# Kernel tuning notes

Measured on AMD Instinct MI355X. Metric: run time of the kernel, lower is better.

Reference implementation:

```python
import jax, jax.numpy as jnp
import numpy as np

IMG = 448; P = 16; C = 3; D = 512; DC = 8; DS = 4
NH = IMG // P            # 28 patches per side
NPATCH = NH * NH         # 784
PDIM = C * P * P         # 768
BATCH = 32
EPS = 1e-5


def setup_inputs() -> dict:
    key = jax.random.key(0)
    ks = jax.random.split(key, 10)
    def lin(k, fan_in, shape):
        bound = 1.0 / np.sqrt(fan_in)
        return jax.random.uniform(k, shape, jnp.float32, -bound, bound)
    return {
        "images": jax.random.normal(ks[0], (BATCH, C, IMG, IMG), jnp.float32),
        "W_patch": lin(ks[1], PDIM, (PDIM, D)),
        "b_patch": jnp.zeros((D,), jnp.float32),
        "pos_embed": jax.random.normal(ks[2], (1, NPATCH, D), jnp.float32) * 0.02,
        "W_coord": lin(ks[3], D, (D, DC)),
        "b_coord": jnp.zeros((DC,), jnp.float32),
        "W_spinor": lin(ks[4], D, (D, DS)),
        "b_spinor": jnp.zeros((DS,), jnp.float32),
        "W_embed": lin(ks[5], DC, (DC, D)),
        "b_embed": jnp.zeros((D,), jnp.float32),
        "ln_gamma": jnp.ones((D,), jnp.float32),
        "ln_beta": jnp.zeros((D,), jnp.float32),
        "W_out": lin(ks[6], D, (D, D)),
        "b_out": jnp.zeros((D,), jnp.float32),
    }


def reference(images, W_patch, b_patch, pos_embed, W_coord, b_coord,
              W_spinor, b_spinor, W_embed, b_embed,
              ln_gamma, ln_beta, W_out, b_out):
    B = images.shape[0]
    # patchify == F.unfold(kernel=stride=P).transpose(1,2):
    # patches[b, bh*NH+bw, c*P*P + i*P + j] = images[b, c, bh*P+i, bw*P+j]
    patches = images.reshape(B, C, NH, P, NH, P)
    patches = patches.transpose(0, 2, 4, 1, 3, 5).reshape(B, NPATCH, PDIM)
    # patch embed + positional embedding  -> (B, NPATCH, D)
    x = patches @ W_patch + b_patch + pos_embed
    # manifold projection: coords (B,N,DC), spinor (B,N,DS)
    coords = x @ W_coord + b_coord
    spinor = x @ W_spinor + b_spinor
    # K0 scalar bilinear: psi^T psi -> (B, N)
    K0 = jnp.sum(spinor * spinor, axis=-1)
    # embed back from manifold coords -> (B, N, D)
    x_manifold = coords @ W_embed + b_embed
    # K0-modulated remix + residual
    x_enh = x_manifold * K0[..., None] + x
    # output projection: LayerNorm -> Linear
    mu = jnp.mean(x_enh, axis=-1, keepdims=True)
    var = jnp.mean(jnp.square(x_enh - mu), axis=-1, keepdims=True)
    x_norm = (x_enh - mu) * jax.lax.rsqrt(var + EPS) * ln_gamma + ln_beta
    return x_norm @ W_out + b_out
```

## Files before the change

kernel.cpp:

```cpp
#include <hip/hip_runtime.h>
#include <hip/hip_bf16.h>
#include <stdint.h>


typedef __bf16 bf16_t;
typedef bf16_t bf16x8 __attribute__((ext_vector_type(8)));
typedef bf16_t bf16x4 __attribute__((ext_vector_type(4)));
typedef float  f32x4  __attribute__((ext_vector_type(4)));

#define IMG     448
#define PSZ     16
#define NHP     28
#define NPATCH  784
#define PDIM    768
#define DMODEL  512
#define MROWS   25088

__device__ __forceinline__ void gload16(void* lds, const void* g) {
  __builtin_amdgcn_global_load_lds(
      (__attribute__((address_space(1))) void*)(uintptr_t)g,
      (__attribute__((address_space(3))) void*)lds,
      16, 0, 0);
}

__global__ __launch_bounds__(256) void prep_patchify(
    const float* __restrict__ Wp, const float* __restrict__ Wo,
    const float* __restrict__ Wc, const float* __restrict__ Ws,
    const float* __restrict__ images,
    bf16_t* __restrict__ WpT, bf16_t* __restrict__ WoT,
    bf16_t* __restrict__ Wcsg, bf16_t* __restrict__ Apat)
{
  __shared__ __align__(16) char shmem[64 * 65 * 4];
  const int tid = threadIdx.x;
  const int blk = blockIdx.x;

  if (blk == 160) {
    for (int idx = tid; idx < 8192; idx += 256) {
      const int r = idx >> 9, n = idx & 511;
      float v = 0.f;
      if (r < 8)       v = Wc[n * 8 + r];
      else if (r < 12) v = Ws[n * 4 + (r - 8)];
      Wcsg[idx] = (bf16_t)v;
    }
    return;
  }

  if (blk < 160) {
    float (*t)[65] = (float(*)[65])shmem;
    const float* src;  bf16_t* dst;  int K, N, bx, by;
    if (blk < 96) { src = Wp; dst = WpT; K = PDIM;   N = DMODEL;
                    bx = (blk & 7) * 64;        by = (blk >> 3) * 64; }
    else          { src = Wo; dst = WoT; K = DMODEL; N = DMODEL;
                    bx = ((blk - 96) & 7) * 64; by = ((blk - 96) >> 3) * 64; }
    const int tx = tid & 63, ty = tid >> 6;
    #pragma unroll
    for (int r = ty; r < 64; r += 4)
      t[r][tx] = src[(size_t)(by + r) * N + (bx + tx)];
    __syncthreads();
    #pragma unroll
    for (int r = ty; r < 64; r += 4)
      dst[(size_t)(bx + r) * K + (by + tx)] = (bf16_t)t[tx][r];
    return;
  }

  bf16_t (*t)[456] = (bf16_t(*)[456])shmem;
  const int bid = blk - 161;
  const int b = bid / 84, rem = bid % 84;
  const int c = rem / 28, ph = rem % 28;
  const float* src = images + ((size_t)(b * 3 + c) * IMG + ph * PSZ) * IMG;

  #pragma unroll
  for (int idx = tid; idx < 16 * 112; idx += 256) {
    const int i = idx / 112, x4 = idx % 112;
    const float4 v = *(const float4*)(src + (size_t)i * IMG + x4 * 4);
    bf16x4 w;
    w[0] = (bf16_t)v.x; w[1] = (bf16_t)v.y; w[2] = (bf16_t)v.z; w[3] = (bf16_t)v.w;
    *(bf16x4*)&t[i][x4 * 4] = w;
  }
  __syncthreads();

  const size_t mbase = (size_t)b * NPATCH + (size_t)ph * NHP;
  #pragma unroll
  for (int idx = tid; idx < 28 * 64; idx += 256) {
    const int pw = idx >> 6, e = idx & 63;
    const int i = e >> 2, j4 = e & 3;
    const bf16x4 w = *(const bf16x4*)&t[i][pw * 16 + j4 * 4];
    *(bf16x4*)&Apat[(mbase + pw) * PDIM + c * 256 + i * 16 + j4 * 4] = w;
  }
}

template<int KDIM, int EPI>
__global__ __launch_bounds__(256, 6) void gemm_bf16(
    const bf16_t* __restrict__ A, const bf16_t* __restrict__ BT,
    const float* __restrict__ bias, const float* __restrict__ pos,
    void* __restrict__ outp)
{
  __shared__ bf16_t As[64 * 64];
  __shared__ bf16_t Bs[128 * 64];
  constexpr int NT = KDIM / 64;

  const int tid  = threadIdx.x;
  const int orig = blockIdx.x;
  const int wg   = (orig & 7) * 196 + (orig >> 3);
  const int n0   = (wg & 3) * 128;
  const int m0   = (wg >> 2) * 64;

  const int wave = tid >> 6, lane = tid & 63;

  const int ra = lane >> 3;
  const int ca = (lane & 7) ^ ra;
  const bf16_t* ag = A  + (size_t)(m0 + wave * 8 + ra) * KDIM + ca * 8;
  const bf16_t* bg = BT + (size_t)(n0 + wave * 8 + ra) * KDIM + ca * 8;
  bf16_t* al0 = As + (wave * 8) * 64;
  bf16_t* al1 = As + (wave * 8 + 32) * 64;
  bf16_t* bl0 = Bs + (wave * 8) * 64;
  bf16_t* bl1 = Bs + (wave * 8 + 32) * 64;
  bf16_t* bl2 = Bs + (wave * 8 + 64) * 64;
  bf16_t* bl3 = Bs + (wave * 8 + 96) * 64;

  const int wm = (wave >> 1) * 32;
  const int wn = (wave & 1) * 64;
  const int lr = lane & 15;
  const int lt = lane >> 4;

  f32x4 acc[2][4] = {};

  for (int t = 0; t < NT; ++t) {
    const int k0 = t * 64;
    __syncthreads();
    gload16(al0, ag + k0);
    gload16(al1, ag + 32 * KDIM + k0);
    gload16(bl0, bg + k0);
    gload16(bl1, bg + 32 * KDIM + k0);
    gload16(bl2, bg + 64 * KDIM + k0);
    gload16(bl3, bg + 96 * KDIM + k0);
    __syncthreads();

    #pragma unroll
    for (int ks = 0; ks < 2; ++ks) {
      const int c = ks * 4 + lt;
      bf16x8 af[2], bfr[4];
      #pragma unroll
      for (int i = 0; i < 2; ++i) {
        const int row = wm + i * 16 + lr;
        af[i] = *(const bf16x8*)&As[row * 64 + ((c ^ (row & 7)) * 8)];
      }
      #pragma unroll
      for (int j = 0; j < 4; ++j) {
        const int row = wn + j * 16 + lr;
        bfr[j] = *(const bf16x8*)&Bs[row * 64 + ((c ^ (row & 7)) * 8)];
      }
      #pragma unroll
      for (int i = 0; i < 2; ++i)
        #pragma unroll
        for (int j = 0; j < 4; ++j)
          acc[i][j] = __builtin_amdgcn_mfma_f32_16x16x32_bf16(af[i], bfr[j], acc[i][j], 0, 0, 0);
    }
  }

  const int q4 = lt << 2;
  const int colb = n0 + wn;
  #pragma unroll
  for (int i = 0; i < 2; ++i) {
    #pragma unroll
    for (int r = 0; r < 4; ++r) {
      const int mm = m0 + wm + i * 16 + q4 + r;
      if (EPI == 0) {
        const int pp = mm % NPATCH;
        const float* pe = pos + (size_t)pp * DMODEL;
        bf16_t* orow = (bf16_t*)outp + (size_t)mm * DMODEL;
        #pragma unroll
        for (int j = 0; j < 4; ++j) {
          const int nn = colb + j * 16 + lr;
          orow[nn] = (bf16_t)(acc[i][j][r] + bias[nn] + pe[nn]);
        }
      } else {
        float* orow = (float*)outp + (size_t)mm * DMODEL;
        #pragma unroll
        for (int j = 0; j < 4; ++j) {
          const int nn = colb + j * 16 + lr;
          orow[nn] = acc[i][j][r] + bias[nn];
        }
      }
    }
  }
}

__global__ __launch_bounds__(256) void manifold_v6(
    bf16_t* __restrict__ x, const bf16_t* __restrict__ Wcsg,
    const float* __restrict__ b_coord, const float* __restrict__ b_spinor,
    const float* __restrict__ We, const float* __restrict__ be,
    const float* __restrict__ gamma, const float* __restrict__ beta)
{
  __shared__ float pbuf[2][2][16][12];

  const int tid  = threadIdx.x;
  const int w    = tid >> 6;
  const int lane = tid & 63;
  const int rg   = w & 1;
  const int kh   = w >> 1;
  const int lr   = lane & 15;
  const int lk   = (lane >> 4) << 3;
  const int q4   = (lane >> 4) << 2;
  const size_t mbase = (size_t)blockIdx.x * 32;

  const bf16_t* xrow = x + (mbase + rg * 16 + lr) * DMODEL + kh * 256 + lk;
  const bf16_t* wrow = Wcsg + lr * DMODEL + kh * 256 + lk;
  f32x4 acc1 = {0.f, 0.f, 0.f, 0.f};
  #pragma unroll
  for (int ks = 0; ks < 8; ++ks) {
    const bf16x8 bf = *(const bf16x8*)(xrow + ks * 32);
    const bf16x8 wf = *(const bf16x8*)(wrow + ks * 32);
    acc1 = __builtin_amdgcn_mfma_f32_16x16x32_bf16(wf, bf, acc1, 0, 0, 0);
  }
  if (q4 < 12) {
    #pragma unroll
    for (int r = 0; r < 4; ++r) pbuf[kh][rg][lr][q4 + r] = acc1[r];
  }
  __syncthreads();

  const int n0 = lane * 8;
  f32x4 wlo[8], whi[8];
  #pragma unroll
  for (int dc = 0; dc < 8; ++dc) {
    wlo[dc] = *(const f32x4*)&We[dc * DMODEL + n0];
    whi[dc] = *(const f32x4*)&We[dc * DMODEL + n0 + 4];
  }
  const f32x4 beL = *(const f32x4*)&be[n0];
  const f32x4 beH = *(const f32x4*)&be[n0 + 4];
  const f32x4 gL  = *(const f32x4*)&gamma[n0];
  const f32x4 gH  = *(const f32x4*)&gamma[n0 + 4];
  const f32x4 btL = *(const f32x4*)&beta[n0];
  const f32x4 btH = *(const f32x4*)&beta[n0 + 4];
  float bc[8], bs[4];
  #pragma unroll
  for (int dc = 0; dc < 8; ++dc) bc[dc] = b_coord[dc];
  #pragma unroll
  for (int ds = 0; ds < 4; ++ds) bs[ds] = b_spinor[ds];

  #pragma unroll 2
  for (int rr = 0; rr < 8; ++rr) {
    const int rloc = w * 8 + rr;
    const int rg2  = rloc >> 4, r16 = rloc & 15;
    const float* p0 = &pbuf[0][rg2][r16][0];
    const float* p1 = &pbuf[1][rg2][r16][0];
    float c[8];
    #pragma unroll
    for (int dc = 0; dc < 8; ++dc) c[dc] = p0[dc] + p1[dc] + bc[dc];
    float k0 = 0.f;
    #pragma unroll
    for (int ds = 0; ds < 4; ++ds) {
      const float s = p0[8 + ds] + p1[8 + ds] + bs[ds];
      k0 += s * s;
    }

    const size_t row = mbase + rloc;
    const bf16x8 xv = *(const bf16x8*)(x + row * DMODEL + n0);

    float v[8];
    float s1 = 0.f, s2 = 0.f;
    #pragma unroll
    for (int e = 0; e < 4; ++e) {
      float xm = beL[e];
      #pragma unroll
      for (int dc = 0; dc < 8; ++dc) xm += c[dc] * wlo[dc][e];
      const float vv = xm * k0 + (float)xv[e];
      v[e] = vv; s1 += vv; s2 += vv * vv;
    }
    #pragma unroll
    for (int e = 0; e < 4; ++e) {
      float xm = beH[e];
      #pragma unroll
      for (int dc = 0; dc < 8; ++dc) xm += c[dc] * whi[dc][e];
      const float vv = xm * k0 + (float)xv[4 + e];
      v[4 + e] = vv; s1 += vv; s2 += vv * vv;
    }

    #pragma unroll
    for (int off = 1; off <= 32; off <<= 1) {
      s1 += __shfl_xor(s1, off, 64);
      s2 += __shfl_xor(s2, off, 64);
    }
    const float mu  = s1 * (1.f / 512.f);
    const float var = s2 * (1.f / 512.f) - mu * mu;
    const float rs  = rsqrtf(var + 1e-5f);

    bf16x8 o;
    #pragma unroll
    for (int e = 0; e < 4; ++e) {
      o[e]     = (bf16_t)((v[e]     - mu) * rs * gL[e] + btL[e]);
      o[4 + e] = (bf16_t)((v[4 + e] - mu) * rs * gH[e] + btH[e]);
    }
    *(bf16x8*)(x + row * DMODEL + n0) = o;
  }
}

extern "C" void kernel_launch(void* const* d_in, const int* in_sizes, int n_in,
                              void* d_out, int out_size, void* d_ws, size_t ws_size,
                              hipStream_t stream)
{
  const float* images    = (const float*)d_in[0];
  const float* W_patch   = (const float*)d_in[1];
  const float* b_patch   = (const float*)d_in[2];
  const float* pos_embed = (const float*)d_in[3];
  const float* W_coord   = (const float*)d_in[4];
  const float* b_coord   = (const float*)d_in[5];
  const float* W_spinor  = (const float*)d_in[6];
  const float* b_spinor  = (const float*)d_in[7];
  const float* W_embed   = (const float*)d_in[8];
  const float* b_embed   = (const float*)d_in[9];
  const float* ln_gamma  = (const float*)d_in[10];
  const float* ln_beta   = (const float*)d_in[11];
  const float* W_out     = (const float*)d_in[12];
  const float* b_out     = (const float*)d_in[13];
  float* out = (float*)d_out;

  const size_t SZ_APAT = (size_t)MROWS * PDIM * 2;
  const size_t SZ_X    = (size_t)MROWS * DMODEL * 2;
  const size_t SZ_WPT  = (size_t)DMODEL * PDIM * 2;
  const size_t SZ_WOT  = (size_t)DMODEL * DMODEL * 2;

  char* ws = (char*)d_ws;
  char* p  = ws;
  bf16_t* Apat = (bf16_t*)p;   p += SZ_APAT;
  bf16_t* x    = (bf16_t*)p;   p += SZ_X;
  bf16_t* WpT  = (bf16_t*)p;   p += SZ_WPT;
  bf16_t* WoT  = (bf16_t*)p;   p += SZ_WOT;
  bf16_t* Wcsg = (bf16_t*)p;

  hipLaunchKernelGGL(prep_patchify, dim3(161 + 32 * 3 * 28), dim3(256), 0, stream,
                     W_patch, W_out, W_coord, W_spinor, images,
                     WpT, WoT, Wcsg, Apat);

  hipLaunchKernelGGL((gemm_bf16<PDIM, 0>), dim3(1568), dim3(256), 0, stream,
                     Apat, WpT, b_patch, pos_embed, (void*)x);

  hipLaunchKernelGGL(manifold_v6, dim3(MROWS / 32), dim3(256), 0, stream,
                     x, Wcsg, b_coord, b_spinor, W_embed, b_embed, ln_gamma, ln_beta);

  hipLaunchKernelGGL((gemm_bf16<DMODEL, 1>), dim3(1568), dim3(256), 0, stream,
                     x, WoT, b_out, (const float*)nullptr, (void*)out);
}
```

Baseline: 102.3 us.

## Restructure GEMM loop sync and split manifold rows across four K-slices

In the GEMM, the first tile's global-to-LDS loads are now issued before the loop, and the next tile's loads are issued after compute, behind a barrier. This is still single-buffered, so the loads do not truly overlap the MFMA work, and the loop ordering is mostly the same. The manifold kernel now handles 16 rows per block instead of 32, with each of four waves reducing a quarter of K, which doubles the grid to increase parallelism. Each block now does less work per launch and reloads the per-block weights (We, gamma, beta) more often.

```diff
diff --git a/kernel.cpp b/kernel.cpp
--- a/kernel.cpp
+++ b/kernel.cpp
@@ -125,15 +125,17 @@
 
   f32x4 acc[2][4] = {};
 
-  for (int t = 0; t < NT; ++t) {
-    const int k0 = t * 64;
-    __syncthreads();
+  auto STAGE = [&](int k0) {
     gload16(al0, ag + k0);
     gload16(al1, ag + 32 * KDIM + k0);
     gload16(bl0, bg + k0);
     gload16(bl1, bg + 32 * KDIM + k0);
     gload16(bl2, bg + 64 * KDIM + k0);
     gload16(bl3, bg + 96 * KDIM + k0);
+  };
+
+  STAGE(0);
+  for (int t = 0; t < NT; ++t) {
     __syncthreads();
 
     #pragma unroll
@@ -155,6 +157,11 @@
         #pragma unroll
         for (int j = 0; j < 4; ++j)
           acc[i][j] = __builtin_amdgcn_mfma_f32_16x16x32_bf16(af[i], bfr[j], acc[i][j], 0, 0, 0);
+    }
+
+    if (t + 1 < NT) {
+      __syncthreads();
+      STAGE((t + 1) * 64);
     }
   }
 
@@ -186,36 +193,34 @@
   }
 }
 
-__global__ __launch_bounds__(256) void manifold_v6(
+__global__ __launch_bounds__(256) void manifold_v7(
     bf16_t* __restrict__ x, const bf16_t* __restrict__ Wcsg,
     const float* __restrict__ b_coord, const float* __restrict__ b_spinor,
     const float* __restrict__ We, const float* __restrict__ be,
     const float* __restrict__ gamma, const float* __restrict__ beta)
 {
-  __shared__ float pbuf[2][2][16][12];
+  __shared__ float pbuf[4][16][12];
 
   const int tid  = threadIdx.x;
   const int w    = tid >> 6;
   const int lane = tid & 63;
-  const int rg   = w & 1;
-  const int kh   = w >> 1;
   const int lr   = lane & 15;
   const int lk   = (lane >> 4) << 3;
   const int q4   = (lane >> 4) << 2;
-  const size_t mbase = (size_t)blockIdx.x * 32;
-
-  const bf16_t* xrow = x + (mbase + rg * 16 + lr) * DMODEL + kh * 256 + lk;
-  const bf16_t* wrow = Wcsg + lr * DMODEL + kh * 256 + lk;
+  const size_t mbase = (size_t)blockIdx.x * 16;
+
+  const bf16_t* xrow = x + (mbase + lr) * DMODEL + w * 128 + lk;
+  const bf16_t* wrow = Wcsg + lr * DMODEL + w * 128 + lk;
   f32x4 acc1 = {0.f, 0.f, 0.f, 0.f};
   #pragma unroll
-  for (int ks = 0; ks < 8; ++ks) {
+  for (int ks = 0; ks < 4; ++ks) {
     const bf16x8 bf = *(const bf16x8*)(xrow + ks * 32);
     const bf16x8 wf = *(const bf16x8*)(wrow + ks * 32);
     acc1 = __builtin_amdgcn_mfma_f32_16x16x32_bf16(wf, bf, acc1, 0, 0, 0);
   }
   if (q4 < 12) {
     #pragma unroll
-    for (int r = 0; r < 4; ++r) pbuf[kh][rg][lr][q4 + r] = acc1[r];
+    for (int r = 0; r < 4; ++r) pbuf[w][lr][q4 + r] = acc1[r];
   }
   __syncthreads();
 
@@ -238,19 +243,21 @@
   #pragma unroll
   for (int ds = 0; ds < 4; ++ds) bs[ds] = b_spinor[ds];
 
-  #pragma unroll 2
-  for (int rr = 0; rr < 8; ++rr) {
-    const int rloc = w * 8 + rr;
-    const int rg2  = rloc >> 4, r16 = rloc & 15;
-    const float* p0 = &pbuf[0][rg2][r16][0];
-    const float* p1 = &pbuf[1][rg2][r16][0];
+  #pragma unroll
+  for (int rr = 0; rr < 4; ++rr) {
+    const int rloc = w * 4 + rr;
+    const float* p0 = &pbuf[0][rloc][0];
+    const float* p1 = &pbuf[1][rloc][0];
+    const float* p2 = &pbuf[2][rloc][0];
+    const float* p3 = &pbuf[3][rloc][0];
     float c[8];
     #pragma unroll
-    for (int dc = 0; dc < 8; ++dc) c[dc] = p0[dc] + p1[dc] + bc[dc];
+    for (int dc = 0; dc < 8; ++dc)
+      c[dc] = ((p0[dc] + p1[dc]) + (p2[dc] + p3[dc])) + bc[dc];
     float k0 = 0.f;
     #pragma unroll
     for (int ds = 0; ds < 4; ++ds) {
-      const float s = p0[8 + ds] + p1[8 + ds] + bs[ds];
+      const float s = ((p0[8 + ds] + p1[8 + ds]) + (p2[8 + ds] + p3[8 + ds])) + bs[ds];
       k0 += s * s;
     }
 
@@ -335,7 +342,7 @@
   hipLaunchKernelGGL((gemm_bf16<PDIM, 0>), dim3(1568), dim3(256), 0, stream,
                      Apat, WpT, b_patch, pos_embed, (void*)x);
 
-  hipLaunchKernelGGL(manifold_v6, dim3(MROWS / 32), dim3(256), 0, stream,
+  hipLaunchKernelGGL(manifold_v7, dim3(MROWS / 16), dim3(256), 0, stream,
                      x, Wcsg, b_coord, b_spinor, W_embed, b_embed, ln_gamma, ln_beta);
 
   hipLaunchKernelGGL((gemm_bf16<DMODEL, 1>), dim3(1568), dim3(256), 0, stream,
```

Result: no change. 101.0 us (-1.3%).
